# Kernel optimization log

Measured on AMD Instinct MI355X. Metric: run time of the kernel, lower is better.

Reference implementation:

```python
import jax, jax.numpy as jnp
import numpy as np
import math

K = 10  # args.k, hardcoded in order_topk/fast_topk

def sinusoid_pe(seq_len, d_model, dtype=jnp.float32):
    # PositionalEmbedding: pe[:,0::2]=sin(pos*div), pe[:,1::2]=cos(pos*div)
    pos = jnp.arange(seq_len, dtype=jnp.float32)[:, None]
    div = jnp.exp(jnp.arange(0, d_model, 2, dtype=jnp.float32) * (-math.log(10000.0) / d_model))
    ang = pos * div  # [S, d_model//2]
    pe = jnp.zeros((seq_len, d_model), dtype=jnp.float32)
    pe = pe.at[:, 0::2].set(jnp.sin(ang)).at[:, 1::2].set(jnp.cos(ang))
    return pe.astype(dtype)


def setup_inputs() -> dict:
    key = jax.random.key(0)
    ks = jax.random.split(key, 5)
    B, D, S = 128, 512, 512
    scale1 = 1.0 / math.sqrt(2 * D)
    scale2 = 1.0 / math.sqrt(D)
    return {
        "x": jax.random.normal(ks[0], (B, D, S), dtype=jnp.float32),
        "w1": jax.random.normal(ks[1], (2 * D, D), dtype=jnp.float32) * scale1,
        "b1": jax.random.normal(ks[2], (D,), dtype=jnp.float32) * scale1,
        "w2": jax.random.normal(ks[3], (D, 1), dtype=jnp.float32) * scale2,
        "b2": jax.random.normal(ks[4], (1,), dtype=jnp.float32) * scale2,
    }


def reference(x, w1, b1, w2, b2):
    # x: [B, D, S] -> feature: [B, S, D]  (Sampler: x = x.transpose(-1,-2))
    feat = jnp.swapaxes(x, -1, -2)
    B, S, D = feat.shape
    # shot == 1 branch: per-video mean over tokens, broadcast over seq
    info_g = jnp.broadcast_to(feat.mean(axis=-2, keepdims=True), feat.shape)
    h = jnp.concatenate([feat, info_g], axis=-1)  # [B, S, 2D]
    # evaluator: PositionalEmbedding(1024) -> Linear(1024,512) -> ReLU -> Linear(512,1)
    h = h + sinusoid_pe(S, 2 * D, h.dtype)[None]
    score = jax.nn.relu(jnp.einsum('bsf,fd->bsd', h, w1) + b1)
    score = (jnp.einsum('bsd,do->bso', score, w2) + b2)[..., 0]  # [B, S]
    mn = score.min(axis=1, keepdims=True)
    mx = score.max(axis=1, keepdims=True)
    norm_score = (score - mn) / (mx - mn + 1e-4)
    # fast_topk (eval path): top-k indices, sorted ascending, one-hot selection
    _, idx = jax.lax.top_k(norm_score, K)      # [B, K]
    idx = jnp.sort(idx, axis=-1)
    # torch: one_hot -> [B,K,S], .transpose(-1,-2) -> [B,S,K], then indices.transpose(-1,-2) -> [B,K,S]
    indices = jax.nn.one_hot(idx, S, dtype=feat.dtype)  # [B, K, S]
    selected_feature = jnp.einsum('bks,bsd->bkd', indices, feat)  # bmm gather
    return indices, selected_feature, feat
```

## Files before the change

### kernel.cpp

```cpp
#include <hip/hip_runtime.h>
#include <math.h>

#define B 128
#define D 512
#define S 512
#define TOPK 10

typedef short bf16x8 __attribute__((ext_vector_type(8)));
typedef unsigned short u16x8 __attribute__((ext_vector_type(8)));
typedef float f32x4 __attribute__((ext_vector_type(4)));
typedef short short4v __attribute__((ext_vector_type(4)));


__global__ void zero_kernel(float* __restrict__ p) {
    p[blockIdx.x * 256 + threadIdx.x] = 0.0f;
}

__global__ __launch_bounds__(256) void transpose_mean_kernel(
    const float* __restrict__ x, float* __restrict__ feat, float* __restrict__ g) {
    __shared__ float tile[64 * 65];
    int b = blockIdx.z;
    int s0 = blockIdx.x * 64, d0 = blockIdx.y * 64;
    int t = threadIdx.x;
    int ty = t >> 4, tx = t & 15;
    const float4* x4 = (const float4*)(x + (size_t)b * D * S);
    float psum[4];
#pragma unroll
    for (int q = 0; q < 4; ++q) {
        int d = ty + 16 * q;
        float4 v = x4[(size_t)(d0 + d) * (S / 4) + (s0 >> 2) + tx];
        tile[d + (4 * tx + 0) * 65] = v.x;
        tile[d + (4 * tx + 1) * 65] = v.y;
        tile[d + (4 * tx + 2) * 65] = v.z;
        tile[d + (4 * tx + 3) * 65] = v.w;
        float sm = (v.x + v.y) + (v.z + v.w);
#pragma unroll
        for (int off = 8; off; off >>= 1) sm += __shfl_down(sm, off, 16);
        psum[q] = sm;
    }
    if (tx == 0) {
#pragma unroll
        for (int q = 0; q < 4; ++q)
            atomicAdd(&g[b * D + d0 + ty + 16 * q], psum[q] * (1.0f / S));
    }
    __syncthreads();
    float4* f4 = (float4*)(feat + (size_t)b * S * D);
#pragma unroll
    for (int q = 0; q < 4; ++q) {
        int s = ty + 16 * q;
        float4 o;
        o.x = tile[(4 * tx + 0) + s * 65];
        o.y = tile[(4 * tx + 1) + s * 65];
        o.z = tile[(4 * tx + 2) + s * 65];
        o.w = tile[(4 * tx + 3) + s * 65];
        f4[(size_t)(s0 + s) * (D / 4) + (d0 >> 2) + tx] = o;
    }
}

__device__ __forceinline__ unsigned splitf(float f) {
    unsigned u = __float_as_uint(f);
    unsigned rb = u + 0x7FFFu + ((u >> 16) & 1u);
    float hf = __uint_as_float(rb & 0xFFFF0000u);
    unsigned u2 = __float_as_uint(f - hf);
    return (rb >> 16) | (u2 & 0xFFFF0000u);
}

__device__ __forceinline__ size_t w1t_base(int d, int k) {
    return (size_t)(((d >> 8) * 32 + (k >> 5)) * 4 + ((k >> 3) & 3)) * 4096 +
           (size_t)(d & 255) * 16 + (k & 7);
}

__global__ void pe_kernel(ushort* __restrict__ peh, ushort* __restrict__ pel) {
    int s = blockIdx.x, t = threadIdx.x;
#pragma unroll
    for (int q = 0; q < 2; ++q) {
        int i = t + 256 * q;
        float ei = expf((float)(2 * i) * -0.0089944730195f);
        float ang = (float)s * ei;
        float sv = sinf(ang), cv = cosf(ang);
        unsigned ps = splitf(sv), pc = splitf(cv);
        size_t base = (size_t)s * 1024 + 2 * i;
        peh[base] = (ushort)(ps & 0xFFFFu);
        peh[base + 1] = (ushort)(pc & 0xFFFFu);
        pel[base] = (ushort)(ps >> 16);
        pel[base + 1] = (ushort)(pc >> 16);
    }
}

__global__ void w1split_kernel(const float* __restrict__ w1, ushort* __restrict__ w1tsw) {
    int rp = blockIdx.x;
    int tt = blockIdx.y;
    int m = threadIdx.x;
    int d = rp * 256 + m;
    int hs = (m >> 2) & 1;
    ushort* out = w1tsw + (size_t)(rp * 32 + tt) * 16384 + (size_t)m * 16;
#pragma unroll
    for (int c = 0; c < 4; ++c) {
        u16x8 hi, lo;
#pragma unroll
        for (int j = 0; j < 8; ++j) {
            unsigned p = splitf(w1[(size_t)(tt * 32 + c * 8 + j) * D + d]);
            hi[j] = (ushort)(p & 0xFFFFu);
            lo[j] = (ushort)(p >> 16);
        }
        *(u16x8*)(out + c * 4096 + hs * 8) = hi;
        *(u16x8*)(out + c * 4096 + (hs ^ 1) * 8) = lo;
    }
}

#define CP 40
__global__ __launch_bounds__(256) void c1_mfma(
    const ushort* __restrict__ peh, const ushort* __restrict__ pel,
    const ushort* __restrict__ w1tsw, const float* __restrict__ b1,
    float* __restrict__ C1) {
    __shared__ short sAh[64 * CP];
    __shared__ short sAl[64 * CP];
    __shared__ short sBh[64 * CP];
    __shared__ short sBl[64 * CP];
    int t = threadIdx.x;
    int d0 = blockIdx.x * 64, s0 = blockIdx.y * 64;
    int w = t >> 6, l = t & 63, lc = l & 15, lg = l >> 4;
    int tm = t >> 2, tk = (t & 3) * 8;
    int bhs = (tm >> 2) & 1;
    f32x4 acc[4] = {};
    for (int k0 = 0; k0 < 1024; k0 += 32) {
        __syncthreads();
        *(bf16x8*)(sAh + tm * CP + tk) = *(const bf16x8*)(peh + (size_t)(s0 + tm) * 1024 + k0 + tk);
        *(bf16x8*)(sAl + tm * CP + tk) = *(const bf16x8*)(pel + (size_t)(s0 + tm) * 1024 + k0 + tk);
        size_t boff = w1t_base(d0 + tm, k0 + tk);
        *(bf16x8*)(sBh + tm * CP + tk) = *(const bf16x8*)(w1tsw + boff + bhs * 8);
        *(bf16x8*)(sBl + tm * CP + tk) = *(const bf16x8*)(w1tsw + boff + (bhs ^ 1) * 8);
        __syncthreads();
        int m = w * 16 + lc;
        bf16x8 ah = *(const bf16x8*)(sAh + m * CP + lg * 8);
        bf16x8 al = *(const bf16x8*)(sAl + m * CP + lg * 8);
#pragma unroll
        for (int j = 0; j < 4; ++j) {
            int n = j * 16 + lc;
            bf16x8 bh = *(const bf16x8*)(sBh + n * CP + lg * 8);
            bf16x8 bl = *(const bf16x8*)(sBl + n * CP + lg * 8);
            acc[j] = __builtin_amdgcn_mfma_f32_16x16x32_bf16(ah, bh, acc[j], 0, 0, 0);
            acc[j] = __builtin_amdgcn_mfma_f32_16x16x32_bf16(ah, bl, acc[j], 0, 0, 0);
            acc[j] = __builtin_amdgcn_mfma_f32_16x16x32_bf16(al, bh, acc[j], 0, 0, 0);
        }
    }
#pragma unroll
    for (int j = 0; j < 4; ++j)
#pragma unroll
        for (int reg = 0; reg < 4; ++reg) {
            int sg = s0 + w * 16 + lg * 4 + reg;
            int dg = d0 + j * 16 + lc;
            C1[(size_t)sg * D + dg] = acc[j][reg] + b1[dg];
        }
}

__global__ void gterm_kernel(const float* __restrict__ g, const float* __restrict__ w1,
                             float* __restrict__ gterm) {
    int b = blockIdx.x;
    int d = blockIdx.y * 256 + threadIdx.x;
    int kc = blockIdx.z * 128;
    const float* gb = g + b * D + kc;
    float a0 = 0.f, a1 = 0.f, a2 = 0.f, a3 = 0.f;
    for (int k = 0; k < 128; k += 4) {
        a0 += gb[k + 0] * w1[(size_t)(D + kc + k + 0) * D + d];
        a1 += gb[k + 1] * w1[(size_t)(D + kc + k + 1) * D + d];
        a2 += gb[k + 2] * w1[(size_t)(D + kc + k + 2) * D + d];
        a3 += gb[k + 3] * w1[(size_t)(D + kc + k + 3) * D + d];
    }
    atomicAdd(&gterm[b * D + d], (a0 + a1) + (a2 + a3));
}

__device__ __forceinline__ void gload16(const void* src, void* dst) {
    __builtin_amdgcn_global_load_lds((const __attribute__((address_space(1))) void*)src,
                                     (__attribute__((address_space(3))) void*)dst, 16, 0, 0);
}

__device__ __forceinline__ void split_write(short* sAbuf, int am, int ahalf,
                                            float4 a0, float4 a1, float4 a2, float4 a3) {
    int hs = (am >> 2) & 1;
#pragma unroll
    for (int cc = 0; cc < 2; ++cc) {
        float e0, e1, e2, e3, e4, e5, e6, e7;
        if (cc == 0) {
            e0 = a0.x; e1 = a0.y; e2 = a0.z; e3 = a0.w;
            e4 = a1.x; e5 = a1.y; e6 = a1.z; e7 = a1.w;
        } else {
            e0 = a2.x; e1 = a2.y; e2 = a2.z; e3 = a2.w;
            e4 = a3.x; e5 = a3.y; e6 = a3.z; e7 = a3.w;
        }
        unsigned p0 = splitf(e0), p1 = splitf(e1), p2 = splitf(e2), p3 = splitf(e3);
        unsigned p4 = splitf(e4), p5 = splitf(e5), p6 = splitf(e6), p7 = splitf(e7);
        u16x8 hi, lo;
        hi[0] = (ushort)(p0 & 0xFFFFu); lo[0] = (ushort)(p0 >> 16);
        hi[1] = (ushort)(p1 & 0xFFFFu); lo[1] = (ushort)(p1 >> 16);
        hi[2] = (ushort)(p2 & 0xFFFFu); lo[2] = (ushort)(p2 >> 16);
        hi[3] = (ushort)(p3 & 0xFFFFu); lo[3] = (ushort)(p3 >> 16);
        hi[4] = (ushort)(p4 & 0xFFFFu); lo[4] = (ushort)(p4 >> 16);
        hi[5] = (ushort)(p5 & 0xFFFFu); lo[5] = (ushort)(p5 >> 16);
        hi[6] = (ushort)(p6 & 0xFFFFu); lo[6] = (ushort)(p6 >> 16);
        hi[7] = (ushort)(p7 & 0xFFFFu); lo[7] = (ushort)(p7 >> 16);
        short* dst = sAbuf + (size_t)(2 * ahalf + cc) * 4096 + (size_t)am * 16;
        *(u16x8*)(dst + hs * 8) = hi;
        *(u16x8*)(dst + (hs ^ 1) * 8) = lo;
    }
}

__global__ __launch_bounds__(512, 2) void gemm_mfma(
    const float* __restrict__ feat, const ushort* __restrict__ w1tsw,
    const float* __restrict__ w2, const float* __restrict__ gterm,
    const float* __restrict__ C1, float* __restrict__ score) {
    __shared__ short sA[2][4][256][16];
    __shared__ short sB[2][4][256][16];
    int t = threadIdx.x;
    int id = (int)blockIdx.x;
    int lid = (id & 7) * 64 + (id >> 3);
    int rp = lid >> 1, cp = lid & 1;
    int row0 = rp << 8;
    int d0 = cp << 8;
    int b = row0 >> 9;

    int am = t & 255, ahalf = t >> 8;
    const float4* asrc = (const float4*)(feat + (size_t)(row0 + am) * D + ahalf * 16);
    const ushort* btile = w1tsw + (size_t)(cp * 32) * 16384;
    int wv = t >> 6, l = t & 63, lc = l & 15, lg = l >> 4;
    int wr = wv >> 1, wc = wv & 1;
    int wbase = (t & ~63);
    int hs = (lc >> 2) & 1;
    int oh = hs * 8, ol = (hs ^ 1) * 8;

    f32x4 acc[4][8] = {};

    {
        float4 a0 = asrc[0], a1 = asrc[1], a2 = asrc[2], a3 = asrc[3];
#pragma unroll
        for (int q = 0; q < 4; ++q)
            gload16(btile + (size_t)(q * 512 + t) * 8,
                    &sB[0][0][0][0] + (size_t)(q * 512 + wbase) * 8);
        split_write(&sA[0][0][0][0], am, ahalf, a0, a1, a2, a3);
    }
    __syncthreads();

    for (int ts = 0; ts < 16; ++ts) {
        int cur = ts & 1, nxt = cur ^ 1;
        float4 a0, a1, a2, a3;
        if (ts < 15) {
            a0 = asrc[(ts + 1) * 8 + 0];
            a1 = asrc[(ts + 1) * 8 + 1];
            a2 = asrc[(ts + 1) * 8 + 2];
            a3 = asrc[(ts + 1) * 8 + 3];
#pragma unroll
            for (int q = 0; q < 4; ++q)
                gload16(btile + (size_t)(ts + 1) * 16384 + (size_t)(q * 512 + t) * 8,
                        &sB[nxt][0][0][0] + (size_t)(q * 512 + wbase) * 8);
        }
        bf16x8 ahf[4], alf[4];
#pragma unroll
        for (int i = 0; i < 4; ++i) {
            const short* ap = &sA[cur][lg][wr * 64 + i * 16 + lc][0];
            ahf[i] = *(const bf16x8*)(ap + oh);
            alf[i] = *(const bf16x8*)(ap + ol);
        }
        __builtin_amdgcn_s_setprio(1);
#pragma unroll
        for (int j = 0; j < 8; ++j) {
            const short* bp = &sB[cur][lg][wc * 128 + j * 16 + lc][0];
            bf16x8 bh = *(const bf16x8*)(bp + oh);
            bf16x8 bl = *(const bf16x8*)(bp + ol);
#pragma unroll
            for (int i = 0; i < 4; ++i) {
                acc[i][j] = __builtin_amdgcn_mfma_f32_16x16x32_bf16(ahf[i], bh, acc[i][j], 0, 0, 0);
                acc[i][j] = __builtin_amdgcn_mfma_f32_16x16x32_bf16(ahf[i], bl, acc[i][j], 0, 0, 0);
                acc[i][j] = __builtin_amdgcn_mfma_f32_16x16x32_bf16(alf[i], bh, acc[i][j], 0, 0, 0);
            }
        }
        __builtin_amdgcn_s_setprio(0);
        if (ts < 15) split_write(&sA[nxt][0][0][0], am, ahalf, a0, a1, a2, a3);
        __syncthreads();
    }

    float w2v[8], gt[8];
#pragma unroll
    for (int j = 0; j < 8; ++j) {
        int d = d0 + wc * 128 + j * 16 + lc;
        w2v[j] = w2[d];
        gt[j] = gterm[b * D + d];
    }
#pragma unroll
    for (int i = 0; i < 4; ++i)
#pragma unroll
        for (int reg = 0; reg < 4; ++reg) {
            int srow = row0 + wr * 64 + i * 16 + lg * 4 + reg;
            int s = srow & 511;
            float part = 0.f;
#pragma unroll
            for (int j = 0; j < 8; ++j) {
                int d = d0 + wc * 128 + j * 16 + lc;
                float z = acc[i][j][reg] + gt[j] + C1[(size_t)s * D + d];
                part += w2v[j] * fmaxf(z, 0.f);
            }
#pragma unroll
            for (int off = 8; off; off >>= 1) part += __shfl_down(part, off, 16);
            if (lc == 0) atomicAdd(&score[srow], part);
        }
}

__global__ void topk_kernel(const float* __restrict__ score, const float* __restrict__ feat,
                            float* __restrict__ out_ind, float* __restrict__ out_sel) {
    __shared__ float work[512];
    __shared__ float wvv[8];
    __shared__ int wii[8];
    __shared__ int topi[TOPK];
    int b = blockIdx.x, t = threadIdx.x;
    work[t] = score[b * S + t];
    __syncthreads();
    for (int it = 0; it < TOPK; ++it) {
        float v = work[t];
        int i = t;
#pragma unroll
        for (int off = 32; off; off >>= 1) {
            float ov = __shfl_down(v, off);
            int oi = __shfl_down(i, off);
            if (ov > v || (ov == v && oi < i)) { v = ov; i = oi; }
        }
        if ((t & 63) == 0) { wvv[t >> 6] = v; wii[t >> 6] = i; }
        __syncthreads();
        if (t == 0) {
            float bv = wvv[0];
            int bi = wii[0];
            for (int w = 1; w < 8; ++w)
                if (wvv[w] > bv || (wvv[w] == bv && wii[w] < bi)) { bv = wvv[w]; bi = wii[w]; }
            topi[it] = bi;
            work[bi] = -INFINITY;
        }
        __syncthreads();
    }
    if (t == 0) {
        for (int a = 1; a < TOPK; ++a) {
            int key = topi[a];
            int c = a - 1;
            while (c >= 0 && topi[c] > key) { topi[c + 1] = topi[c]; --c; }
            topi[c + 1] = key;
        }
    }
    __syncthreads();
    float* oi_b = out_ind + (size_t)b * TOPK * S;
#pragma unroll
    for (int k = 0; k < TOPK; ++k) oi_b[k * S + t] = 0.0f;
    __syncthreads();
    if (t < TOPK) oi_b[t * S + topi[t]] = 1.0f;
    float* os_b = out_sel + (size_t)b * TOPK * D;
    const float* fb = feat + (size_t)b * S * D;
#pragma unroll
    for (int k = 0; k < TOPK; ++k) os_b[k * D + t] = fb[(size_t)topi[k] * D + t];
}

extern "C" void kernel_launch(void* const* d_in, const int* in_sizes, int n_in,
                              void* d_out, int out_size, void* d_ws, size_t ws_size,
                              hipStream_t stream) {
    const float* x  = (const float*)d_in[0];
    const float* w1 = (const float*)d_in[1];
    const float* b1 = (const float*)d_in[2];
    const float* w2 = (const float*)d_in[3];

    float* out = (float*)d_out;
    float* out_ind = out;
    float* out_sel = out + (size_t)B * TOPK * S;
    float* feat    = out + 2 * (size_t)B * TOPK * S;

    float* ws      = (float*)d_ws;
    float* g       = ws;
    float* gterm   = ws + 65536;
    float* score   = ws + 131072;
    float* C1      = ws + 196608;
    ushort* w1tsw  = (ushort*)(ws + 458752);
    ushort* peh    = (ushort*)(ws + 983040);
    ushort* pel    = (ushort*)(ws + 1245184);

    zero_kernel<<<768, 256, 0, stream>>>(ws);
    transpose_mean_kernel<<<dim3(8, 8, B), 256, 0, stream>>>(x, feat, g);
    gterm_kernel<<<dim3(B, 2, 4), 256, 0, stream>>>(g, w1, gterm);
    pe_kernel<<<S, 256, 0, stream>>>(peh, pel);
    w1split_kernel<<<dim3(2, 32), 256, 0, stream>>>(w1, w1tsw);
    c1_mfma<<<dim3(8, 8), 256, 0, stream>>>(peh, pel, w1tsw, b1, C1);
    gemm_mfma<<<512, 512, 0, stream>>>(feat, w1tsw, w2, gterm, C1, score);
    topk_kernel<<<B, 512, 0, stream>>>(score, feat, out_ind, out_sel);
}
```

Before: 425.0 us.

## Split B-tile loads into four phases interleaved with MFMA work in main GEMM

Reorganizes the pre-split w1 layout into per-phase 64-row chunks so each K-step's B tile can be loaded in four quarter pieces. The main GEMM loop now issues one async global-to-LDS load per phase between MFMA groups, using explicit s_barrier and vmcnt/lgkmcnt waits instead of a single __syncthreads. It also peels off the last iteration. The goal is to spread global loads and barrier stalls across the compute, at the cost of more barriers per iteration and hand-managed wait counts that must stay correct.

```diff
diff --git a/kernel.cpp b/kernel.cpp
--- a/kernel.cpp
+++ b/kernel.cpp
@@ -9,7 +9,6 @@
 typedef short bf16x8 __attribute__((ext_vector_type(8)));
 typedef unsigned short u16x8 __attribute__((ext_vector_type(8)));
 typedef float f32x4 __attribute__((ext_vector_type(4)));
-typedef short short4v __attribute__((ext_vector_type(4)));
 
 
 __global__ void zero_kernel(float* __restrict__ p) {
@@ -65,9 +64,13 @@
     return (rb >> 16) | (u2 & 0xFFFF0000u);
 }
 
-__device__ __forceinline__ size_t w1t_base(int d, int k) {
-    return (size_t)(((d >> 8) * 32 + (k >> 5)) * 4 + ((k >> 3) & 3)) * 4096 +
-           (size_t)(d & 255) * 16 + (k & 7);
+__device__ __forceinline__ size_t w1t_addr(int d, int k, int& hs) {
+    int cp = d >> 8, dd = d & 255;
+    int p = (dd & 127) >> 5;
+    int rg = ((dd >> 7) & 1) * 32 + (dd & 31);
+    hs = (rg >> 2) & 1;
+    return (size_t)(((cp * 32 + (k >> 5)) * 4 + p) * 4 + ((k >> 3) & 3)) * 1024 +
+           rg * 16 + (k & 7);
 }
 
 __global__ void pe_kernel(ushort* __restrict__ peh, ushort* __restrict__ pel) {
@@ -88,23 +91,25 @@
 }
 
 __global__ void w1split_kernel(const float* __restrict__ w1, ushort* __restrict__ w1tsw) {
-    int rp = blockIdx.x;
-    int tt = blockIdx.y;
-    int m = threadIdx.x;
-    int d = rp * 256 + m;
-    int hs = (m >> 2) & 1;
-    ushort* out = w1tsw + (size_t)(rp * 32 + tt) * 16384 + (size_t)m * 16;
-#pragma unroll
-    for (int c = 0; c < 4; ++c) {
+    int cp = blockIdx.x;
+    int ts = blockIdx.y;
+    int t = threadIdx.x;
+    int p = t >> 6, rg = t & 63;
+    int dd = (rg < 32) ? (32 * p + rg) : (128 + 32 * p + (rg - 32));
+    int d = cp * 256 + dd;
+    int hsw = (rg >> 2) & 1;
+    ushort* out = w1tsw + (size_t)(((cp * 32 + ts) * 4 + p) * 4) * 1024 + rg * 16;
+#pragma unroll
+    for (int kc = 0; kc < 4; ++kc) {
         u16x8 hi, lo;
 #pragma unroll
-        for (int j = 0; j < 8; ++j) {
-            unsigned p = splitf(w1[(size_t)(tt * 32 + c * 8 + j) * D + d]);
-            hi[j] = (ushort)(p & 0xFFFFu);
-            lo[j] = (ushort)(p >> 16);
-        }
-        *(u16x8*)(out + c * 4096 + hs * 8) = hi;
-        *(u16x8*)(out + c * 4096 + (hs ^ 1) * 8) = lo;
+        for (int e = 0; e < 8; ++e) {
+            unsigned pk = splitf(w1[(size_t)(ts * 32 + kc * 8 + e) * D + d]);
+            hi[e] = (ushort)(pk & 0xFFFFu);
+            lo[e] = (ushort)(pk >> 16);
+        }
+        *(u16x8*)(out + kc * 1024 + hsw * 8) = hi;
+        *(u16x8*)(out + kc * 1024 + (hsw ^ 1) * 8) = lo;
     }
 }
 
@@ -121,13 +126,13 @@
     int d0 = blockIdx.x * 64, s0 = blockIdx.y * 64;
     int w = t >> 6, l = t & 63, lc = l & 15, lg = l >> 4;
     int tm = t >> 2, tk = (t & 3) * 8;
-    int bhs = (tm >> 2) & 1;
     f32x4 acc[4] = {};
     for (int k0 = 0; k0 < 1024; k0 += 32) {
         __syncthreads();
         *(bf16x8*)(sAh + tm * CP + tk) = *(const bf16x8*)(peh + (size_t)(s0 + tm) * 1024 + k0 + tk);
         *(bf16x8*)(sAl + tm * CP + tk) = *(const bf16x8*)(pel + (size_t)(s0 + tm) * 1024 + k0 + tk);
-        size_t boff = w1t_base(d0 + tm, k0 + tk);
+        int bhs;
+        size_t boff = w1t_addr(d0 + tm, k0 + tk, bhs);
         *(bf16x8*)(sBh + tm * CP + tk) = *(const bf16x8*)(w1tsw + boff + bhs * 8);
         *(bf16x8*)(sBl + tm * CP + tk) = *(const bf16x8*)(w1tsw + boff + (bhs ^ 1) * 8);
         __syncthreads();
@@ -177,7 +182,7 @@
 
 __device__ __forceinline__ void split_write(short* sAbuf, int am, int ahalf,
                                             float4 a0, float4 a1, float4 a2, float4 a3) {
-    int hs = (am >> 2) & 1;
+    int hsw = (am >> 2) & 1;
 #pragma unroll
     for (int cc = 0; cc < 2; ++cc) {
         float e0, e1, e2, e3, e4, e5, e6, e7;
@@ -200,17 +205,41 @@
         hi[6] = (ushort)(p6 & 0xFFFFu); lo[6] = (ushort)(p6 >> 16);
         hi[7] = (ushort)(p7 & 0xFFFFu); lo[7] = (ushort)(p7 >> 16);
         short* dst = sAbuf + (size_t)(2 * ahalf + cc) * 4096 + (size_t)am * 16;
-        *(u16x8*)(dst + hs * 8) = hi;
-        *(u16x8*)(dst + (hs ^ 1) * 8) = lo;
-    }
-}
+        *(u16x8*)(dst + hsw * 8) = hi;
+        *(u16x8*)(dst + (hsw ^ 1) * 8) = lo;
+    }
+}
+
+#define BARR() __builtin_amdgcn_s_barrier()
+#define LGKM0() asm volatile("s_waitcnt lgkmcnt(0)" ::: "memory")
+#define VMW(N) asm volatile("s_waitcnt vmcnt(" #N ")" ::: "memory")
+
+#define PHASE(BCUR, P, JA, JB)                                                        \
+    {                                                                                 \
+        const short* bp_ = (BCUR) + (P) * 4096 + bbase;                               \
+        bf16x8 bh0_ = *(const bf16x8*)(bp_ + oh), bl0_ = *(const bf16x8*)(bp_ + ol);  \
+        bf16x8 bh1_ = *(const bf16x8*)(bp_ + 256 + oh),                               \
+               bl1_ = *(const bf16x8*)(bp_ + 256 + ol);                               \
+        BARR();                                                                       \
+        LGKM0();                                                                      \
+        __builtin_amdgcn_s_setprio(1);                                                \
+        _Pragma("unroll") for (int i_ = 0; i_ < 4; ++i_) {                            \
+            acc[i_][JA] = __builtin_amdgcn_mfma_f32_16x16x32_bf16(ahf[i_], bh0_, acc[i_][JA], 0, 0, 0); \
+            acc[i_][JA] = __builtin_amdgcn_mfma_f32_16x16x32_bf16(ahf[i_], bl0_, acc[i_][JA], 0, 0, 0); \
+            acc[i_][JA] = __builtin_amdgcn_mfma_f32_16x16x32_bf16(alf[i_], bh0_, acc[i_][JA], 0, 0, 0); \
+            acc[i_][JB] = __builtin_amdgcn_mfma_f32_16x16x32_bf16(ahf[i_], bh1_, acc[i_][JB], 0, 0, 0); \
+            acc[i_][JB] = __builtin_amdgcn_mfma_f32_16x16x32_bf16(ahf[i_], bl1_, acc[i_][JB], 0, 0, 0); \
+            acc[i_][JB] = __builtin_amdgcn_mfma_f32_16x16x32_bf16(alf[i_], bh1_, acc[i_][JB], 0, 0, 0); \
+        }                                                                             \
+        __builtin_amdgcn_s_setprio(0);                                                \
+    }
 
 __global__ __launch_bounds__(512, 2) void gemm_mfma(
     const float* __restrict__ feat, const ushort* __restrict__ w1tsw,
     const float* __restrict__ w2, const float* __restrict__ gterm,
     const float* __restrict__ C1, float* __restrict__ score) {
     __shared__ short sA[2][4][256][16];
-    __shared__ short sB[2][4][256][16];
+    __shared__ short sB[2][4][4][64][16];
     int t = threadIdx.x;
     int id = (int)blockIdx.x;
     int lid = (id & 7) * 64 + (id >> 3);
@@ -228,54 +257,82 @@
     int hs = (lc >> 2) & 1;
     int oh = hs * 8, ol = (hs ^ 1) * 8;
 
+    short* sA0 = &sA[0][0][0][0];
+    short* sA1 = &sA[1][0][0][0];
+    short* sB0 = &sB[0][0][0][0][0];
+    short* sB1 = &sB[1][0][0][0][0];
+    int abase = lg * 4096 + (wr * 64 + lc) * 16;
+    int bbase = lg * 1024 + (wc * 32 + lc) * 16;
+
     f32x4 acc[4][8] = {};
 
     {
         float4 a0 = asrc[0], a1 = asrc[1], a2 = asrc[2], a3 = asrc[3];
 #pragma unroll
-        for (int q = 0; q < 4; ++q)
-            gload16(btile + (size_t)(q * 512 + t) * 8,
-                    &sB[0][0][0][0] + (size_t)(q * 512 + wbase) * 8);
-        split_write(&sA[0][0][0][0], am, ahalf, a0, a1, a2, a3);
-    }
-    __syncthreads();
-
-    for (int ts = 0; ts < 16; ++ts) {
-        int cur = ts & 1, nxt = cur ^ 1;
-        float4 a0, a1, a2, a3;
-        if (ts < 15) {
-            a0 = asrc[(ts + 1) * 8 + 0];
-            a1 = asrc[(ts + 1) * 8 + 1];
-            a2 = asrc[(ts + 1) * 8 + 2];
-            a3 = asrc[(ts + 1) * 8 + 3];
-#pragma unroll
-            for (int q = 0; q < 4; ++q)
-                gload16(btile + (size_t)(ts + 1) * 16384 + (size_t)(q * 512 + t) * 8,
-                        &sB[nxt][0][0][0] + (size_t)(q * 512 + wbase) * 8);
-        }
+        for (int p = 0; p < 4; ++p)
+            gload16(btile + (size_t)p * 4096 + (size_t)t * 8, sB0 + p * 4096 + wbase * 8);
+        split_write(sA0, am, ahalf, a0, a1, a2, a3);
+        LGKM0();
+        VMW(3);
+        BARR();
+    }
+
+    for (int ts = 0; ts < 15; ++ts) {
+        const short* Ac = (ts & 1) ? sA1 : sA0;
+        short* An = (ts & 1) ? sA0 : sA1;
+        const short* Bc = (ts & 1) ? sB1 : sB0;
+        short* Bn = (ts & 1) ? sB0 : sB1;
+        const ushort* bsrc = btile + (size_t)(ts + 1) * 16384;
+
+        float4 a0 = asrc[(ts + 1) * 8 + 0], a1 = asrc[(ts + 1) * 8 + 1],
+               a2 = asrc[(ts + 1) * 8 + 2], a3 = asrc[(ts + 1) * 8 + 3];
+        gload16(bsrc + (size_t)t * 8, Bn + wbase * 8);
         bf16x8 ahf[4], alf[4];
 #pragma unroll
         for (int i = 0; i < 4; ++i) {
-            const short* ap = &sA[cur][lg][wr * 64 + i * 16 + lc][0];
+            const short* ap = Ac + abase + i * 256;
             ahf[i] = *(const bf16x8*)(ap + oh);
             alf[i] = *(const bf16x8*)(ap + ol);
         }
-        __builtin_amdgcn_s_setprio(1);
-#pragma unroll
-        for (int j = 0; j < 8; ++j) {
-            const short* bp = &sB[cur][lg][wc * 128 + j * 16 + lc][0];
-            bf16x8 bh = *(const bf16x8*)(bp + oh);
-            bf16x8 bl = *(const bf16x8*)(bp + ol);
-#pragma unroll
-            for (int i = 0; i < 4; ++i) {
-                acc[i][j] = __builtin_amdgcn_mfma_f32_16x16x32_bf16(ahf[i], bh, acc[i][j], 0, 0, 0);
-                acc[i][j] = __builtin_amdgcn_mfma_f32_16x16x32_bf16(ahf[i], bl, acc[i][j], 0, 0, 0);
-                acc[i][j] = __builtin_amdgcn_mfma_f32_16x16x32_bf16(alf[i], bh, acc[i][j], 0, 0, 0);
-            }
-        }
-        __builtin_amdgcn_s_setprio(0);
-        if (ts < 15) split_write(&sA[nxt][0][0][0], am, ahalf, a0, a1, a2, a3);
-        __syncthreads();
+        PHASE(Bc, 0, 0, 1);
+        VMW(7);
+        BARR();
+        gload16(bsrc + 4096 + (size_t)t * 8, Bn + 4096 + wbase * 8);
+        PHASE(Bc, 1, 2, 3);
+        VMW(7);
+        BARR();
+        gload16(bsrc + 8192 + (size_t)t * 8, Bn + 8192 + wbase * 8);
+        PHASE(Bc, 2, 4, 5);
+        VMW(7);
+        BARR();
+        gload16(bsrc + 12288 + (size_t)t * 8, Bn + 12288 + wbase * 8);
+        PHASE(Bc, 3, 6, 7);
+        split_write(An, am, ahalf, a0, a1, a2, a3);
+        LGKM0();
+        VMW(3);
+        BARR();
+    }
+
+    {
+        const short* Ac = sA1;
+        const short* Bc = sB1;
+        bf16x8 ahf[4], alf[4];
+#pragma unroll
+        for (int i = 0; i < 4; ++i) {
+            const short* ap = Ac + abase + i * 256;
+            ahf[i] = *(const bf16x8*)(ap + oh);
+            alf[i] = *(const bf16x8*)(ap + ol);
+        }
+        PHASE(Bc, 0, 0, 1);
+        VMW(2);
+        BARR();
+        PHASE(Bc, 1, 2, 3);
+        VMW(1);
+        BARR();
+        PHASE(Bc, 2, 4, 5);
+        VMW(0);
+        BARR();
+        PHASE(Bc, 3, 6, 7);
     }
 
     float w2v[8], gt[8];
```

Result: slower. 441.9 us (+4.0%).

## Merge preprocessing kernels into two block-dispatched fused launches

Applied to the files above, without the earlier changes.

Transpose/mean, positional-encoding split and w1 split are merged into one launch whose blocks branch on block index. The gterm matvec and the PE×W1 MFMA GEMM are merged into a second launch. gterm now covers the full K range per block from a shared-memory copy of g and stores directly instead of atomically, which lets the zero pass shrink. The goal is to cut launch gaps and let independent small kernels overlap, at the cost of mixing heterogeneous blocks with different resource needs in one launch.

```diff
diff --git a/kernel.cpp b/kernel.cpp
--- a/kernel.cpp
+++ b/kernel.cpp
@@ -9,53 +9,7 @@
 typedef short bf16x8 __attribute__((ext_vector_type(8)));
 typedef unsigned short u16x8 __attribute__((ext_vector_type(8)));
 typedef float f32x4 __attribute__((ext_vector_type(4)));
-typedef short short4v __attribute__((ext_vector_type(4)));
-
-
-__global__ void zero_kernel(float* __restrict__ p) {
-    p[blockIdx.x * 256 + threadIdx.x] = 0.0f;
-}
-
-__global__ __launch_bounds__(256) void transpose_mean_kernel(
-    const float* __restrict__ x, float* __restrict__ feat, float* __restrict__ g) {
-    __shared__ float tile[64 * 65];
-    int b = blockIdx.z;
-    int s0 = blockIdx.x * 64, d0 = blockIdx.y * 64;
-    int t = threadIdx.x;
-    int ty = t >> 4, tx = t & 15;
-    const float4* x4 = (const float4*)(x + (size_t)b * D * S);
-    float psum[4];
-#pragma unroll
-    for (int q = 0; q < 4; ++q) {
-        int d = ty + 16 * q;
-        float4 v = x4[(size_t)(d0 + d) * (S / 4) + (s0 >> 2) + tx];
-        tile[d + (4 * tx + 0) * 65] = v.x;
-        tile[d + (4 * tx + 1) * 65] = v.y;
-        tile[d + (4 * tx + 2) * 65] = v.z;
-        tile[d + (4 * tx + 3) * 65] = v.w;
-        float sm = (v.x + v.y) + (v.z + v.w);
-#pragma unroll
-        for (int off = 8; off; off >>= 1) sm += __shfl_down(sm, off, 16);
-        psum[q] = sm;
-    }
-    if (tx == 0) {
-#pragma unroll
-        for (int q = 0; q < 4; ++q)
-            atomicAdd(&g[b * D + d0 + ty + 16 * q], psum[q] * (1.0f / S));
-    }
-    __syncthreads();
-    float4* f4 = (float4*)(feat + (size_t)b * S * D);
-#pragma unroll
-    for (int q = 0; q < 4; ++q) {
-        int s = ty + 16 * q;
-        float4 o;
-        o.x = tile[(4 * tx + 0) + s * 65];
-        o.y = tile[(4 * tx + 1) + s * 65];
-        o.z = tile[(4 * tx + 2) + s * 65];
-        o.w = tile[(4 * tx + 3) + s * 65];
-        f4[(size_t)(s0 + s) * (D / 4) + (d0 >> 2) + tx] = o;
-    }
-}
+
 
 __device__ __forceinline__ unsigned splitf(float f) {
     unsigned u = __float_as_uint(f);
@@ -70,104 +24,159 @@
            (size_t)(d & 255) * 16 + (k & 7);
 }
 
-__global__ void pe_kernel(ushort* __restrict__ peh, ushort* __restrict__ pel) {
-    int s = blockIdx.x, t = threadIdx.x;
-#pragma unroll
-    for (int q = 0; q < 2; ++q) {
-        int i = t + 256 * q;
-        float ei = expf((float)(2 * i) * -0.0089944730195f);
-        float ang = (float)s * ei;
-        float sv = sinf(ang), cv = cosf(ang);
-        unsigned ps = splitf(sv), pc = splitf(cv);
-        size_t base = (size_t)s * 1024 + 2 * i;
-        peh[base] = (ushort)(ps & 0xFFFFu);
-        peh[base + 1] = (ushort)(pc & 0xFFFFu);
-        pel[base] = (ushort)(ps >> 16);
-        pel[base + 1] = (ushort)(pc >> 16);
-    }
-}
-
-__global__ void w1split_kernel(const float* __restrict__ w1, ushort* __restrict__ w1tsw) {
-    int rp = blockIdx.x;
-    int tt = blockIdx.y;
-    int m = threadIdx.x;
-    int d = rp * 256 + m;
-    int hs = (m >> 2) & 1;
-    ushort* out = w1tsw + (size_t)(rp * 32 + tt) * 16384 + (size_t)m * 16;
-#pragma unroll
-    for (int c = 0; c < 4; ++c) {
-        u16x8 hi, lo;
-#pragma unroll
-        for (int j = 0; j < 8; ++j) {
-            unsigned p = splitf(w1[(size_t)(tt * 32 + c * 8 + j) * D + d]);
-            hi[j] = (ushort)(p & 0xFFFFu);
-            lo[j] = (ushort)(p >> 16);
-        }
-        *(u16x8*)(out + c * 4096 + hs * 8) = hi;
-        *(u16x8*)(out + c * 4096 + (hs ^ 1) * 8) = lo;
+__global__ void zero_kernel(float* __restrict__ p) {
+    p[blockIdx.x * 256 + threadIdx.x] = 0.0f;
+}
+
+__global__ __launch_bounds__(256) void fused_stage1(
+    const float* __restrict__ x, float* __restrict__ feat, float* __restrict__ g,
+    ushort* __restrict__ peh, ushort* __restrict__ pel,
+    const float* __restrict__ w1, ushort* __restrict__ w1tsw) {
+    __shared__ float tile[64 * 65];
+    int bid = (int)blockIdx.x;
+    int t = threadIdx.x;
+
+    if (bid < 8192) {
+        int b = bid >> 6;
+        int s0 = (bid & 7) * 64, d0 = ((bid >> 3) & 7) * 64;
+        int ty = t >> 4, tx = t & 15;
+        const float4* x4 = (const float4*)(x + (size_t)b * D * S);
+        float psum[4];
+#pragma unroll
+        for (int q = 0; q < 4; ++q) {
+            int d = ty + 16 * q;
+            float4 v = x4[(size_t)(d0 + d) * (S / 4) + (s0 >> 2) + tx];
+            tile[d + (4 * tx + 0) * 65] = v.x;
+            tile[d + (4 * tx + 1) * 65] = v.y;
+            tile[d + (4 * tx + 2) * 65] = v.z;
+            tile[d + (4 * tx + 3) * 65] = v.w;
+            float sm = (v.x + v.y) + (v.z + v.w);
+#pragma unroll
+            for (int off = 8; off; off >>= 1) sm += __shfl_down(sm, off, 16);
+            psum[q] = sm;
+        }
+        if (tx == 0) {
+#pragma unroll
+            for (int q = 0; q < 4; ++q)
+                atomicAdd(&g[b * D + d0 + ty + 16 * q], psum[q] * (1.0f / S));
+        }
+        __syncthreads();
+        float4* f4 = (float4*)(feat + (size_t)b * S * D);
+#pragma unroll
+        for (int q = 0; q < 4; ++q) {
+            int s = ty + 16 * q;
+            float4 o;
+            o.x = tile[(4 * tx + 0) + s * 65];
+            o.y = tile[(4 * tx + 1) + s * 65];
+            o.z = tile[(4 * tx + 2) + s * 65];
+            o.w = tile[(4 * tx + 3) + s * 65];
+            f4[(size_t)(s0 + s) * (D / 4) + (d0 >> 2) + tx] = o;
+        }
+    } else if (bid < 8704) {
+        int s = bid - 8192;
+#pragma unroll
+        for (int q = 0; q < 2; ++q) {
+            int i = t + 256 * q;
+            float ei = expf((float)(2 * i) * -0.0089944730195f);
+            float ang = (float)s * ei;
+            float sv = sinf(ang), cv = cosf(ang);
+            unsigned ps = splitf(sv), pc = splitf(cv);
+            size_t base = (size_t)s * 1024 + 2 * i;
+            peh[base] = (ushort)(ps & 0xFFFFu);
+            peh[base + 1] = (ushort)(pc & 0xFFFFu);
+            pel[base] = (ushort)(ps >> 16);
+            pel[base + 1] = (ushort)(pc >> 16);
+        }
+    } else {
+        int id2 = bid - 8704;
+        int rp = id2 & 1, tt = id2 >> 1;
+        int m = t;
+        int d = rp * 256 + m;
+        int hs = (m >> 2) & 1;
+        ushort* outp = w1tsw + (size_t)(rp * 32 + tt) * 16384 + (size_t)m * 16;
+#pragma unroll
+        for (int c = 0; c < 4; ++c) {
+            u16x8 hi, lo;
+#pragma unroll
+            for (int j = 0; j < 8; ++j) {
+                unsigned p = splitf(w1[(size_t)(tt * 32 + c * 8 + j) * D + d]);
+                hi[j] = (ushort)(p & 0xFFFFu);
+                lo[j] = (ushort)(p >> 16);
+            }
+            *(u16x8*)(outp + c * 4096 + hs * 8) = hi;
+            *(u16x8*)(outp + c * 4096 + (hs ^ 1) * 8) = lo;
+        }
     }
 }
 
 #define CP 40
-__global__ __launch_bounds__(256) void c1_mfma(
+__global__ __launch_bounds__(256) void fused_stage2(
+    const float* __restrict__ g, const float* __restrict__ w1, float* __restrict__ gterm,
     const ushort* __restrict__ peh, const ushort* __restrict__ pel,
     const ushort* __restrict__ w1tsw, const float* __restrict__ b1,
     float* __restrict__ C1) {
-    __shared__ short sAh[64 * CP];
-    __shared__ short sAl[64 * CP];
-    __shared__ short sBh[64 * CP];
-    __shared__ short sBl[64 * CP];
+    __shared__ short smemS[4 * 64 * CP];
+    int bid = (int)blockIdx.x;
     int t = threadIdx.x;
-    int d0 = blockIdx.x * 64, s0 = blockIdx.y * 64;
-    int w = t >> 6, l = t & 63, lc = l & 15, lg = l >> 4;
-    int tm = t >> 2, tk = (t & 3) * 8;
-    int bhs = (tm >> 2) & 1;
-    f32x4 acc[4] = {};
-    for (int k0 = 0; k0 < 1024; k0 += 32) {
-        __syncthreads();
-        *(bf16x8*)(sAh + tm * CP + tk) = *(const bf16x8*)(peh + (size_t)(s0 + tm) * 1024 + k0 + tk);
-        *(bf16x8*)(sAl + tm * CP + tk) = *(const bf16x8*)(pel + (size_t)(s0 + tm) * 1024 + k0 + tk);
-        size_t boff = w1t_base(d0 + tm, k0 + tk);
-        *(bf16x8*)(sBh + tm * CP + tk) = *(const bf16x8*)(w1tsw + boff + bhs * 8);
-        *(bf16x8*)(sBl + tm * CP + tk) = *(const bf16x8*)(w1tsw + boff + (bhs ^ 1) * 8);
-        __syncthreads();
-        int m = w * 16 + lc;
-        bf16x8 ah = *(const bf16x8*)(sAh + m * CP + lg * 8);
-        bf16x8 al = *(const bf16x8*)(sAl + m * CP + lg * 8);
-#pragma unroll
-        for (int j = 0; j < 4; ++j) {
-            int n = j * 16 + lc;
-            bf16x8 bh = *(const bf16x8*)(sBh + n * CP + lg * 8);
-            bf16x8 bl = *(const bf16x8*)(sBl + n * CP + lg * 8);
-            acc[j] = __builtin_amdgcn_mfma_f32_16x16x32_bf16(ah, bh, acc[j], 0, 0, 0);
-            acc[j] = __builtin_amdgcn_mfma_f32_16x16x32_bf16(ah, bl, acc[j], 0, 0, 0);
-            acc[j] = __builtin_amdgcn_mfma_f32_16x16x32_bf16(al, bh, acc[j], 0, 0, 0);
-        }
-    }
-#pragma unroll
-    for (int j = 0; j < 4; ++j)
-#pragma unroll
-        for (int reg = 0; reg < 4; ++reg) {
-            int sg = s0 + w * 16 + lg * 4 + reg;
-            int dg = d0 + j * 16 + lc;
-            C1[(size_t)sg * D + dg] = acc[j][reg] + b1[dg];
-        }
-}
-
-__global__ void gterm_kernel(const float* __restrict__ g, const float* __restrict__ w1,
-                             float* __restrict__ gterm) {
-    int b = blockIdx.x;
-    int d = blockIdx.y * 256 + threadIdx.x;
-    int kc = blockIdx.z * 128;
-    const float* gb = g + b * D + kc;
-    float a0 = 0.f, a1 = 0.f, a2 = 0.f, a3 = 0.f;
-    for (int k = 0; k < 128; k += 4) {
-        a0 += gb[k + 0] * w1[(size_t)(D + kc + k + 0) * D + d];
-        a1 += gb[k + 1] * w1[(size_t)(D + kc + k + 1) * D + d];
-        a2 += gb[k + 2] * w1[(size_t)(D + kc + k + 2) * D + d];
-        a3 += gb[k + 3] * w1[(size_t)(D + kc + k + 3) * D + d];
-    }
-    atomicAdd(&gterm[b * D + d], (a0 + a1) + (a2 + a3));
+
+    if (bid < 256) {
+        int b = bid >> 1, half = bid & 1;
+        float* gs = (float*)smemS;
+        gs[t] = g[b * D + t];
+        gs[t + 256] = g[b * D + 256 + t];
+        __syncthreads();
+        int d = half * 256 + t;
+        float a0 = 0.f, a1 = 0.f, a2 = 0.f, a3 = 0.f;
+        for (int k = 0; k < 512; k += 4) {
+            a0 += gs[k + 0] * w1[(size_t)(D + k + 0) * D + d];
+            a1 += gs[k + 1] * w1[(size_t)(D + k + 1) * D + d];
+            a2 += gs[k + 2] * w1[(size_t)(D + k + 2) * D + d];
+            a3 += gs[k + 3] * w1[(size_t)(D + k + 3) * D + d];
+        }
+        gterm[b * D + d] = (a0 + a1) + (a2 + a3);
+    } else {
+        int cid = bid - 256;
+        int d0 = (cid & 7) * 64, s0 = (cid >> 3) * 64;
+        short* sAh = smemS;
+        short* sAl = smemS + 64 * CP;
+        short* sBh = smemS + 2 * 64 * CP;
+        short* sBl = smemS + 3 * 64 * CP;
+        int w = t >> 6, l = t & 63, lc = l & 15, lg = l >> 4;
+        int tm = t >> 2, tk = (t & 3) * 8;
+        int bhs = (tm >> 2) & 1;
+        f32x4 acc[4] = {};
+        for (int k0 = 0; k0 < 1024; k0 += 32) {
+            __syncthreads();
+            *(bf16x8*)(sAh + tm * CP + tk) =
+                *(const bf16x8*)(peh + (size_t)(s0 + tm) * 1024 + k0 + tk);
+            *(bf16x8*)(sAl + tm * CP + tk) =
+                *(const bf16x8*)(pel + (size_t)(s0 + tm) * 1024 + k0 + tk);
+            size_t boff = w1t_base(d0 + tm, k0 + tk);
+            *(bf16x8*)(sBh + tm * CP + tk) = *(const bf16x8*)(w1tsw + boff + bhs * 8);
+            *(bf16x8*)(sBl + tm * CP + tk) = *(const bf16x8*)(w1tsw + boff + (bhs ^ 1) * 8);
+            __syncthreads();
+            int m = w * 16 + lc;
+            bf16x8 ah = *(const bf16x8*)(sAh + m * CP + lg * 8);
+            bf16x8 al = *(const bf16x8*)(sAl + m * CP + lg * 8);
+#pragma unroll
+            for (int j = 0; j < 4; ++j) {
+                int n = j * 16 + lc;
+                bf16x8 bh = *(const bf16x8*)(sBh + n * CP + lg * 8);
+                bf16x8 bl = *(const bf16x8*)(sBl + n * CP + lg * 8);
+                acc[j] = __builtin_amdgcn_mfma_f32_16x16x32_bf16(ah, bh, acc[j], 0, 0, 0);
+                acc[j] = __builtin_amdgcn_mfma_f32_16x16x32_bf16(ah, bl, acc[j], 0, 0, 0);
+                acc[j] = __builtin_amdgcn_mfma_f32_16x16x32_bf16(al, bh, acc[j], 0, 0, 0);
+            }
+        }
+#pragma unroll
+        for (int j = 0; j < 4; ++j)
+#pragma unroll
+            for (int reg = 0; reg < 4; ++reg) {
+                int sg = s0 + w * 16 + lg * 4 + reg;
+                int dg = d0 + j * 16 + lc;
+                C1[(size_t)sg * D + dg] = acc[j][reg] + b1[dg];
+            }
+    }
 }
 
 __device__ __forceinline__ void gload16(const void* src, void* dst) {
@@ -369,19 +378,16 @@
 
     float* ws      = (float*)d_ws;
     float* g       = ws;
-    float* gterm   = ws + 65536;
-    float* score   = ws + 131072;
+    float* score   = ws + 65536;
+    float* gterm   = ws + 131072;
     float* C1      = ws + 196608;
     ushort* w1tsw  = (ushort*)(ws + 458752);
     ushort* peh    = (ushort*)(ws + 983040);
     ushort* pel    = (ushort*)(ws + 1245184);
 
-    zero_kernel<<<768, 256, 0, stream>>>(ws);
-    transpose_mean_kernel<<<dim3(8, 8, B), 256, 0, stream>>>(x, feat, g);
-    gterm_kernel<<<dim3(B, 2, 4), 256, 0, stream>>>(g, w1, gterm);
-    pe_kernel<<<S, 256, 0, stream>>>(peh, pel);
-    w1split_kernel<<<dim3(2, 32), 256, 0, stream>>>(w1, w1tsw);
-    c1_mfma<<<dim3(8, 8), 256, 0, stream>>>(peh, pel, w1tsw, b1, C1);
+    zero_kernel<<<512, 256, 0, stream>>>(ws);
+    fused_stage1<<<8768, 256, 0, stream>>>(x, feat, g, peh, pel, w1, w1tsw);
+    fused_stage2<<<320, 256, 0, stream>>>(g, w1, gterm, peh, pel, w1tsw, b1, C1);
     gemm_mfma<<<512, 512, 0, stream>>>(feat, w1tsw, w2, gterm, C1, score);
     topk_kernel<<<B, 512, 0, stream>>>(score, feat, out_ind, out_sel);
 }
```

After: 414.4 us. 1.03x faster.
